# Optimization experiments

Measured on AMD Instinct MI355X. Metric: run time of the kernel, lower is better.

## Reference

```python
import jax, jax.numpy as jnp
import numpy as np

SCALE_FACTOR = 2  # init kwarg
KERNEL = 1        # kernel=1 -> no Gaussian inpainting of empty cells
EPS = 1e-6


def token2map_agg(x, loc_orig, idx_agg, H, W):
    """Scatter-average aggregated tokens onto a dense [B,C,H,W] map.

    Faithful to token2map_agg_sparse with weight=None, kernel=1:
      each original position i gets feature x[idx_agg[i]] with weight 1,
      scattered to the grid cell of loc_orig[i]; per-cell average with
      denominator (count + 1e-6).
    """
    B, N, C = x.shape
    N0 = loc_orig.shape[1]
    lo = jnp.clip(loc_orig, -1.0, 1.0)
    wh = jnp.array([W, H], dtype=lo.dtype)
    # normalized [-1,1] -> pixel coords, round-half-even like torch.round
    px = jnp.round(0.5 * (lo + 1.0) * wh - 0.5).astype(jnp.int32)
    ix = jnp.clip(px[..., 0], 0, W - 1)
    iy = jnp.clip(px[..., 1], 0, H - 1)
    seg = (iy * W + ix + jnp.arange(B, dtype=jnp.int32)[:, None] * (H * W)).reshape(-1)  # [B*N0]
    # gather token feature for each original position: [B, N0, C]
    feats = jnp.take_along_axis(x, idx_agg[..., None].astype(jnp.int32), axis=1)
    # scatter features and counts together in one segment_sum
    src = jnp.concatenate([feats, jnp.ones_like(feats[..., :1])], axis=-1).reshape(B * N0, C + 1)
    agg = jax.ops.segment_sum(src, seg, num_segments=B * H * W)  # [B*H*W, C+1]
    out = agg[:, :C] / (agg[:, C:] + EPS)
    return out.reshape(B, H, W, C).transpose(0, 3, 1, 2)  # [B,C,H,W]


def setup_inputs() -> dict:
    key = jax.random.key(0)
    k1, k2, k3, k4 = jax.random.split(key, 4)
    B, N, C = 8, 1024, 128
    N0 = 16384  # 128*128 original grid positions
    x = jax.random.normal(k1, (B, N, C), dtype=jnp.float32)
    loc = jax.random.uniform(k2, (B, N, 2), dtype=jnp.float32, minval=-1.0, maxval=1.0)
    loc_orig = jax.random.uniform(k3, (B, N0, 2), dtype=jnp.float32, minval=-1.0, maxval=1.0)
    idx_agg = jax.random.randint(k4, (B, N0), 0, N, dtype=jnp.int32)
    return {"x": x, "loc": loc, "loc_orig": loc_orig, "idx_agg": idx_agg,
            "map_h": 128, "map_w": 128}


def reference(x, loc, loc_orig, idx_agg, map_h, map_w):
    B, N, C = x.shape
    N0 = idx_agg.shape[1]
    scale_orig = (N0 // N) ** 0.5  # static python value
    if SCALE_FACTOR <= scale_orig:
        h, w = int(map_h * SCALE_FACTOR), int(map_w * SCALE_FACTOR)
        out = token2map_agg(x, loc_orig, idx_agg, h, w)
    else:
        h, w = int(map_h * scale_orig), int(map_w * scale_orig)
        out = token2map_agg(x, loc_orig, idx_agg, h, w)
        h, w = int(map_h * SCALE_FACTOR), int(map_w * SCALE_FACTOR)
        out = jax.image.resize(out, (B, C, h, w), method="bilinear")
    return out
```

## Files before the change

kernel.cpp:

```cpp
#include <hip/hip_runtime.h>

constexpr int B  = 8;
constexpr int N  = 1024;
constexpr int C  = 128;
constexpr int N0 = 16384;
constexpr int HH = 256;
constexpr int WW = 256;
constexpr int HW = HH * WW;
constexpr int NPTS = B * N0;

constexpr int CPG  = 32;
constexpr int GPB  = HW / CPG;
constexpr int NGRP = B * GPB;
constexpr int CAP  = 96;

constexpr int ROW  = CPG + 4;
constexpr int ACC_WORDS = C * ROW;

__device__ __forceinline__ int cell_of(float lx, float ly) {
    lx = fminf(fmaxf(lx, -1.0f), 1.0f);
    ly = fminf(fmaxf(ly, -1.0f), 1.0f);
    float pxf = rintf(0.5f * (lx + 1.0f) * 256.0f - 0.5f);
    float pyf = rintf(0.5f * (ly + 1.0f) * 256.0f - 0.5f);
    int ix = (int)pxf; ix = ix < 0 ? 0 : (ix > WW - 1 ? WW - 1 : ix);
    int iy = (int)pyf; iy = iy < 0 ? 0 : (iy > HH - 1 ? HH - 1 : iy);
    return iy * WW + ix;
}

__global__ void bucket_kernel(const float* __restrict__ loc_orig,
                              const int* __restrict__ idx_agg,
                              int* __restrict__ cursor,
                              int* __restrict__ bucket) {
    int p = blockIdx.x * blockDim.x + threadIdx.x;
    if (p >= NPTS) return;
    float2 l = ((const float2*)loc_orig)[p];
    int b = p >> 14;
    int cell = cell_of(l.x, l.y);
    int g = b * GPB + (cell >> 5);
    int pos = atomicAdd(cursor + g, 1);
    if (pos < CAP) bucket[g * CAP + pos] = ((cell & 31) << 10) | idx_agg[p];
}

__global__ __launch_bounds__(256) void gather_kernel(
        const float* __restrict__ x,
        const int* __restrict__ cursor,
        const int* __restrict__ bucket,
        float* __restrict__ out) {
    __shared__ float acc[ACC_WORDS];
    __shared__ float scale[CPG];
    __shared__ int   recs[CAP];
    __shared__ int   cnt_s;

    int gid   = blockIdx.x;
    int b     = gid >> 11;
    int cell0 = (gid & 2047) * CPG;
    int tid   = threadIdx.x;
    int wave  = tid >> 6, lane = tid & 63;

    int my_cnt = (tid == 0) ? cursor[gid] : 0;
    int my_rec = (tid < CAP) ? bucket[gid * CAP + tid] : 0;

    float4 z4 = make_float4(0.f, 0.f, 0.f, 0.f);
    for (int i = tid; i < ACC_WORDS / 4; i += 256) ((float4*)acc)[i] = z4;
    if (tid < CPG) scale[tid] = 0.0f;

    if (tid == 0) cnt_s = my_cnt > CAP ? CAP : my_cnt;
    if (tid < CAP) recs[tid] = my_rec;
    __syncthreads();

    int cnt = cnt_s;

    for (int j = wave; j < cnt; j += 4) {
        int e = recs[j];
        int local = e >> 10;
        int tok   = e & 1023;
        float2 v = ((const float2*)(x + (size_t)(b * N + tok) * C))[lane];
        atomicAdd(&acc[(2 * lane)     * ROW + local], v.x);
        atomicAdd(&acc[(2 * lane + 1) * ROW + local], v.y);
        if (lane == 0) atomicAdd(&scale[local], 1.0f);
    }
    __syncthreads();
    if (tid < CPG) scale[tid] = 1.0f / (scale[tid] + 1e-6f);
    __syncthreads();

    int i4 = (tid & 7) * 4;
    int cb = tid >> 3;
    float s0 = scale[i4 + 0], s1 = scale[i4 + 1];
    float s2 = scale[i4 + 2], s3 = scale[i4 + 3];
    float* obase = out + (size_t)b * C * HW + cell0;
    #pragma unroll
    for (int it = 0; it < 4; ++it) {
        int c = it * 32 + cb;
        float4 v = *(const float4*)&acc[c * ROW + i4];
        v.x *= s0; v.y *= s1; v.z *= s2; v.w *= s3;
        *(float4*)(obase + (size_t)c * HW + i4) = v;
    }
}

extern "C" void kernel_launch(void* const* d_in, const int* in_sizes, int n_in,
                              void* d_out, int out_size, void* d_ws, size_t ws_size,
                              hipStream_t stream) {
    const float* x        = (const float*)d_in[0];
    const float* loc_orig = (const float*)d_in[2];
    const int*   idx_agg  = (const int*)d_in[3];
    float* out = (float*)d_out;

    int* cursor = (int*)d_ws;
    int* bucket = cursor + NGRP;

    hipMemsetAsync(cursor, 0, NGRP * sizeof(int), stream);
    bucket_kernel<<<(NPTS + 255) / 256, 256, 0, stream>>>(loc_orig, idx_agg, cursor, bucket);
    gather_kernel<<<NGRP, 256, 0, stream>>>(x, cursor, bucket, out);
}
```

Measured before the change: 354.2 us.

## Process eight cell groups per block with prefetched bucket records

Each gather block now loops over eight consecutive 32-cell groups instead of one. It reuses the shared accumulator, clearing it while writing each group's output, and prefetches the next group's bucket records and count into registers while accumulating the current one. The aim is to cut block launch and setup overhead and to hide bucket load latency. In exchange, parallelism drops to an eighth as many blocks, there is an extra barrier per group, and the launch bounds now request 8 blocks per CU.

```diff
diff --git a/kernel.cpp b/kernel.cpp
--- a/kernel.cpp
+++ b/kernel.cpp
@@ -13,6 +13,9 @@
 constexpr int GPB  = HW / CPG;
 constexpr int NGRP = B * GPB;
 constexpr int CAP  = 96;
+
+constexpr int GPBLK = 8;
+constexpr int NBLK  = NGRP / GPBLK;
 
 constexpr int ROW  = CPG + 4;
 constexpr int ACC_WORDS = C * ROW;
@@ -41,59 +44,71 @@
     if (pos < CAP) bucket[g * CAP + pos] = ((cell & 31) << 10) | idx_agg[p];
 }
 
-__global__ __launch_bounds__(256) void gather_kernel(
+__global__ __launch_bounds__(256, 8) void gather_kernel(
         const float* __restrict__ x,
         const int* __restrict__ cursor,
         const int* __restrict__ bucket,
         float* __restrict__ out) {
     __shared__ float acc[ACC_WORDS];
+    __shared__ float cntf[CPG];
     __shared__ float scale[CPG];
     __shared__ int   recs[CAP];
     __shared__ int   cnt_s;
 
-    int gid   = blockIdx.x;
-    int b     = gid >> 11;
-    int cell0 = (gid & 2047) * CPG;
-    int tid   = threadIdx.x;
-    int wave  = tid >> 6, lane = tid & 63;
+    int g0  = blockIdx.x * GPBLK;
+    int b   = g0 >> 11;
+    int tid = threadIdx.x;
+    int wave = tid >> 6, lane = tid & 63;
 
-    int my_cnt = (tid == 0) ? cursor[gid] : 0;
-    int my_rec = (tid < CAP) ? bucket[gid * CAP + tid] : 0;
+    int r0 = (tid < CAP) ? bucket[g0 * CAP + tid] : 0;
+    int c0 = (tid == 0) ? cursor[g0] : 0;
 
     float4 z4 = make_float4(0.f, 0.f, 0.f, 0.f);
     for (int i = tid; i < ACC_WORDS / 4; i += 256) ((float4*)acc)[i] = z4;
-    if (tid < CPG) scale[tid] = 0.0f;
-
-    if (tid == 0) cnt_s = my_cnt > CAP ? CAP : my_cnt;
-    if (tid < CAP) recs[tid] = my_rec;
+    if (tid < CPG) cntf[tid] = 0.0f;
+    if (tid < CAP) recs[tid] = r0;
+    if (tid == 0) cnt_s = c0 > CAP ? CAP : c0;
     __syncthreads();
 
-    int cnt = cnt_s;
+    for (int k = 0; k < GPBLK; ++k) {
+        int g     = g0 + k;
+        int cell0 = (g & 2047) * CPG;
 
-    for (int j = wave; j < cnt; j += 4) {
-        int e = recs[j];
-        int local = e >> 10;
-        int tok   = e & 1023;
-        float2 v = ((const float2*)(x + (size_t)(b * N + tok) * C))[lane];
-        atomicAdd(&acc[(2 * lane)     * ROW + local], v.x);
-        atomicAdd(&acc[(2 * lane + 1) * ROW + local], v.y);
-        if (lane == 0) atomicAdd(&scale[local], 1.0f);
-    }
-    __syncthreads();
-    if (tid < CPG) scale[tid] = 1.0f / (scale[tid] + 1e-6f);
-    __syncthreads();
+        int gn = (k + 1 < GPBLK) ? g + 1 : g;
+        int r_next = (tid < CAP) ? bucket[gn * CAP + tid] : 0;
+        int c_next = (tid == 0) ? cursor[gn] : 0;
 
-    int i4 = (tid & 7) * 4;
-    int cb = tid >> 3;
-    float s0 = scale[i4 + 0], s1 = scale[i4 + 1];
-    float s2 = scale[i4 + 2], s3 = scale[i4 + 3];
-    float* obase = out + (size_t)b * C * HW + cell0;
-    #pragma unroll
-    for (int it = 0; it < 4; ++it) {
-        int c = it * 32 + cb;
-        float4 v = *(const float4*)&acc[c * ROW + i4];
-        v.x *= s0; v.y *= s1; v.z *= s2; v.w *= s3;
-        *(float4*)(obase + (size_t)c * HW + i4) = v;
+        int cnt = cnt_s;
+        for (int j = wave; j < cnt; j += 4) {
+            int e = recs[j];
+            int local = e >> 10;
+            int tok   = e & 1023;
+            float2 v = ((const float2*)(x + (size_t)(b * N + tok) * C))[lane];
+            atomicAdd(&acc[(2 * lane)     * ROW + local], v.x);
+            atomicAdd(&acc[(2 * lane + 1) * ROW + local], v.y);
+            if (lane == 0) atomicAdd(&cntf[local], 1.0f);
+        }
+        __syncthreads();
+
+        if (tid < CPG) { scale[tid] = 1.0f / (cntf[tid] + 1e-6f); cntf[tid] = 0.0f; }
+        if (tid < CAP) recs[tid] = r_next;
+        if (tid == 0)  cnt_s = c_next > CAP ? CAP : c_next;
+        __syncthreads();
+
+        int i4 = (tid & 7) * 4;
+        int cb = tid >> 3;
+        float s0 = scale[i4 + 0], s1 = scale[i4 + 1];
+        float s2 = scale[i4 + 2], s3 = scale[i4 + 3];
+        float* obase = out + (size_t)b * C * HW + cell0;
+        #pragma unroll
+        for (int it = 0; it < 4; ++it) {
+            int c = it * 32 + cb;
+            float4 v = *(const float4*)&acc[c * ROW + i4];
+            v.x *= s0; v.y *= s1; v.z *= s2; v.w *= s3;
+            *(float4*)(obase + (size_t)c * HW + i4) = v;
+            *(float4*)&acc[c * ROW + i4] = z4;
+        }
+        __syncthreads();
     }
 }
 
@@ -110,5 +125,5 @@
 
     hipMemsetAsync(cursor, 0, NGRP * sizeof(int), stream);
     bucket_kernel<<<(NPTS + 255) / 256, 256, 0, stream>>>(loc_orig, idx_agg, cursor, bucket);
-    gather_kernel<<<NGRP, 256, 0, stream>>>(x, cursor, bucket, out);
+    gather_kernel<<<NBLK, 256, 0, stream>>>(x, cursor, bucket, out);
 }
```

After: 356.6 us. No clear change (+0.7%).
